# Kernel optimization log

Measured on AMD Instinct MI355X. Metric: run time of the kernel, lower is better.

The kernel has to match this reference:

```python
import jax, jax.numpy as jnp
import numpy as np

VOCAB, D, A, H, F = 100000, 128, 128, 4, 128  # embed dim == attention_dim (residual), 4 heads, final_dim
B, L, L2 = 64, 200, 50
NEG = float(-2**32 + 1)


def setup_inputs() -> dict:
    key = jax.random.key(0)
    ks = jax.random.split(key, 12)
    queries = jax.random.randint(ks[0], (B, L), 0, VOCAB)
    keys = jax.random.randint(ks[1], (B, L, L2), 0, VOCAB)
    E = jax.random.normal(ks[2], (VOCAB, D), dtype=jnp.float32) * 0.02
    Wq = jax.random.normal(ks[3], (D, A), dtype=jnp.float32) * (1.0 / np.sqrt(D))
    bq = jnp.zeros((A,), jnp.float32)
    Wk = jax.random.normal(ks[4], (D, A), dtype=jnp.float32) * (1.0 / np.sqrt(D))
    bk = jnp.zeros((A,), jnp.float32)
    Wv = jax.random.normal(ks[5], (D, A), dtype=jnp.float32) * (1.0 / np.sqrt(D))
    bv = jnp.zeros((A,), jnp.float32)
    Wf = jax.random.normal(ks[6], (A, F), dtype=jnp.float32) * (1.0 / np.sqrt(A))
    bf = jnp.zeros((F,), jnp.float32)
    return {"queries": queries, "keys": keys, "E": E, "Wq": Wq, "bq": bq,
            "Wk": Wk, "bk": bk, "Wv": Wv, "bv": bv, "Wf": Wf, "bf": bf}


def reference(queries, keys, E, Wq, bq, Wk, bk, Wv, bv, Wf, bf):
    q_emb = E[queries]                      # [B, L, D]
    k_emb = E[keys]                         # [B, L, L2, D]
    Q = q_emb @ Wq + bq                     # [B, L, A]
    K = k_emb @ Wk + bk                     # [B, L, L2, A]
    V = k_emb @ Wv + bv                     # [B, L, L2, A]
    d = A // H
    Qh = Q.reshape(Q.shape[0], Q.shape[1], H, d)                       # [B, L, H, d]
    Kh = K.reshape(K.shape[0], K.shape[1], K.shape[2], H, d)           # [B, L, L2, H, d]
    Vh = V.reshape(V.shape[0], V.shape[1], V.shape[2], H, d)
    # per-(b,l) query attends over its L2 keys, per head; scale by sqrt(depth)
    scores = jnp.einsum('blhd,blkhd->bhlk', Qh, Kh) / jnp.sqrt(jnp.asarray(d, Q.dtype))
    # padding mask from embedded-key content: sign(|sum_d k_emb|) == 0 -> masked
    key_mask = jnp.sign(jnp.abs(jnp.sum(k_emb, axis=-1)))              # [B, L, L2]
    scores = jnp.where(key_mask[:, None, :, :] == 0, NEG, scores)
    attn = jax.nn.softmax(scores, axis=-1)                             # [B, H, L, L2]
    out = jnp.einsum('bhlk,blkhd->blhd', attn, Vh)
    out = out.reshape(out.shape[0], out.shape[1], A)                   # [B, L, A]
    out = out + q_emb                                                  # residual
    return out @ Wf + bf                                               # [B, L, F]
```

## Files before the change

### kernel.cpp

```cpp
#include <hip/hip_runtime.h>
#include <stdint.h>

#define DN 128
#define AN 128
#define HN 4
#define FN 128
#define L2N 50
#define NPOS (64*200)
#define NEGC (-4294967295.0f)

#define OFF_MTWB 0
#define OFF_GTB  40960
#define OFF_CB   73728
#define OFF_U    74368
#define OFF_R    3351168
#define OFF_PV   4989568

typedef __fp16 half2v __attribute__((ext_vector_type(2)));
typedef __fp16 f16x8  __attribute__((ext_vector_type(8)));
typedef float  f32x4  __attribute__((ext_vector_type(4)));
union frg { uint4 u; f16x8 h; };

__device__ __forceinline__ float dot2(uint32_t a, uint32_t b, float c) {
#if __has_builtin(__builtin_amdgcn_fdot2)
    union { uint32_t u; half2v h; } ca, cb; ca.u = a; cb.u = b;
    return __builtin_amdgcn_fdot2(ca.h, cb.h, c, false);
#else
    union { uint32_t u; _Float16 h[2]; } ca, cb; ca.u = a; cb.u = b;
    return c + (float)ca.h[0]*(float)cb.h[0] + (float)ca.h[1]*(float)cb.h[1];
#endif
}
__device__ __forceinline__ uint32_t packh2(float x, float y) {
    union { _Float16 h[2]; uint32_t u; } c; c.h[0] = (_Float16)x; c.h[1] = (_Float16)y;
    return c.u;
}
__device__ __forceinline__ float lo16f(uint32_t u) {
    union { uint32_t u; _Float16 h[2]; } c; c.u = u; return (float)c.h[0];
}
__device__ __forceinline__ float hi16f(uint32_t u) {
    union { uint32_t u; _Float16 h[2]; } c; c.u = u; return (float)c.h[1];
}

__global__ __launch_bounds__(256) void k0_pre(
    const float* __restrict__ Wq, const float* __restrict__ bq,
    const float* __restrict__ Wk, const float* __restrict__ bk,
    const float* __restrict__ Wv, const float* __restrict__ bv,
    const float* __restrict__ Wf, const float* __restrict__ bfb,
    float* __restrict__ ws)
{
    uint32_t* MTWB = (uint32_t*)ws + OFF_MTWB;
    uint32_t* GTBw = (uint32_t*)ws + OFF_GTB;
    float*    CB   = ws + OFF_CB;
    const int idx = blockIdx.x*256 + threadIdx.x;

    if (idx < 40960) {
        int jj = idx & 3, lane = (idx>>2)&63, kk = (idx>>8)&3, tn = idx>>10;
        int outc = tn*16 + (lane&15);
        int dd2  = kk*16 + (lane>>4)*4 + jj;
        int dd0  = 2*dd2, dd1 = dd0+1;
        float s0, s1;
        if (outc < 512) {
            int h = outc >> 7, d = outc & 127;
            const float* wk = Wk + d*AN + h*32;
            const float* q0 = Wq + dd0*AN + h*32;
            const float* q1 = Wq + dd1*AN + h*32;
            s0 = 0.f; s1 = 0.f;
            #pragma unroll 8
            for (int j = 0; j < 32; ++j) { float w = wk[j]; s0 += q0[j]*w; s1 += q1[j]*w; }
        } else {
            int f = outc - 512;
            s0 = Wf[dd0*FN + f]; s1 = Wf[dd1*FN + f];
        }
        MTWB[idx] = packh2(s0, s1);
    } else if (idx < 73728) {
        int i2 = idx - 40960;
        int jj = i2 & 3, lane = (i2>>2)&63, kk = (i2>>8)&15, tn = i2>>12;
        int f  = tn*16 + (lane&15);
        int j2 = kk*16 + (lane>>4)*4 + jj;
        int hd0 = 2*j2;
        int h = hd0 >> 7, d0 = hd0 & 127, d1 = d0+1;
        const float* v0 = Wv + d0*AN + h*32;
        const float* v1 = Wv + d1*AN + h*32;
        float s0 = 0.f, s1 = 0.f;
        #pragma unroll 8
        for (int a = 0; a < 32; ++a) {
            float wf = Wf[(h*32+a)*FN + f];
            s0 += v0[a]*wf; s1 += v1[a]*wf;
        }
        GTBw[i2] = packh2(s0, s1);
    } else {
        int c = idx - 73728;
        if (c < 512) {
            int h = c >> 7, d = c & 127;
            float s = 0.f;
            #pragma unroll 8
            for (int j = 0; j < 32; ++j) s += Wk[d*AN + h*32 + j]*bq[h*32 + j];
            CB[c] = s;
        } else if (c < 640) {
            int f = c - 512;
            float s = bfb[f];
            for (int a = 0; a < AN; ++a) s += bv[a]*Wf[a*FN + f];
            CB[c] = s;
        }
    }
}

__global__ __launch_bounds__(256) void k1_proj(
    const int* __restrict__ queries, const float* __restrict__ E,
    float* __restrict__ ws)
{
    const uint32_t* MTWB = (const uint32_t*)ws + OFF_MTWB;
    const float*    CB   = ws + OFF_CB;
    uint32_t* U = (uint32_t*)ws + OFF_U;
    float*    R = ws + OFF_R;

    const int t = threadIdx.x, wv = t >> 6, ln = t & 63;
    const int W  = blockIdx.x*4 + wv;
    const int tm = W / 5, g = W - tm*5;
    const int m = ln & 15, q = ln >> 4;
    const int pos0 = tm*16 + q*4;

    const int qidx = queries[tm*16 + m];
    const float* Eq = E + (size_t)qidx * DN;

    frg a[4];
    #pragma unroll
    for (int kk = 0; kk < 4; ++kk) {
        float4 e0 = *(const float4*)(Eq + kk*32 + q*8);
        float4 e1 = *(const float4*)(Eq + kk*32 + q*8 + 4);
        a[kk].u.x = packh2(e0.x, e0.y);
        a[kk].u.y = packh2(e0.z, e0.w);
        a[kk].u.z = packh2(e1.x, e1.y);
        a[kk].u.w = packh2(e1.z, e1.w);
    }

    #pragma unroll 1
    for (int i = 0; i < 8; ++i) {
        const int tn = g*8 + i;
        const float cb = CB[tn*16 + m];
        f32x4 c = {cb, cb, cb, cb};
        #pragma unroll
        for (int kk = 0; kk < 4; ++kk) {
            frg b; b.u = *(const uint4*)(MTWB + ((size_t)(tn*4 + kk)*64 + ln)*4);
            c = __builtin_amdgcn_mfma_f32_16x16x32_f16(a[kk].h, b.h, c, 0, 0, 0);
        }
        if (tn < 32) {
            float p0 = __shfl_xor(c[0], 1);
            float p1 = __shfl_xor(c[1], 1);
            float p2 = __shfl_xor(c[2], 1);
            float p3 = __shfl_xor(c[3], 1);
            if ((ln & 1) == 0) {
                const int ucol = tn*8 + (m >> 1);
                U[(size_t)(pos0+0)*256 + ucol] = packh2(c[0], p0);
                U[(size_t)(pos0+1)*256 + ucol] = packh2(c[1], p1);
                U[(size_t)(pos0+2)*256 + ucol] = packh2(c[2], p2);
                U[(size_t)(pos0+3)*256 + ucol] = packh2(c[3], p3);
            }
        } else {
            const int f = (tn - 32)*16 + m;
            R[(size_t)(pos0+0)*128 + f] = c[0];
            R[(size_t)(pos0+1)*128 + f] = c[1];
            R[(size_t)(pos0+2)*128 + f] = c[2];
            R[(size_t)(pos0+3)*128 + f] = c[3];
        }
    }
}

__global__ __launch_bounds__(128, 2) void k2_attn(
    const int* __restrict__ keys, const float* __restrict__ E,
    float* __restrict__ ws)
{
    __shared__ __align__(16) uint32_t smem[7748];

    const uint32_t* U  = (const uint32_t*)ws + OFF_U;
    uint32_t*       PV = (uint32_t*)ws + OFF_PV;

    const int t = threadIdx.x, wv = t >> 6, ln = t & 63;
    const int pos = blockIdx.x*2 + wv;
    const int n = ln & 15, qd = ln >> 4;
    const int half = ln >> 5;
    const int m32 = ln & 31;

    uint32_t* kT = smem + wv*3400;
    uint32_t* Us = smem + 6800 + wv*272;
    float*    aT = (float*)(smem + 7344 + wv*200);

    const int* kptr = keys + (size_t)pos*L2N;
    const float* Eg = E + 4*m32;

    const int myk = kptr[ln < L2N ? ln : 0];

    uint4 uv = ((const uint4*)(U + (size_t)pos*256))[ln];

    float4 f4[25];
    #pragma unroll
    for (int i = 0; i < 25; ++i) {
        int row = __shfl(myk, 2*i + half);
        f4[i] = *(const float4*)(Eg + (size_t)row*DN);
    }

    *(uint4*)&Us[qd*68 + (n<<2)] = uv;

    frg bfr[4];
    #pragma unroll
    for (int kk = 0; kk < 4; ++kk) {
        if (n < 4) {
            bfr[kk].u = *(const uint4*)&Us[n*68 + kk*16 + (qd<<2)];
        } else if (n == 4) {
            bfr[kk].u.x = 0x3C003C00u; bfr[kk].u.y = 0x3C003C00u;
            bfr[kk].u.z = 0x3C003C00u; bfr[kk].u.w = 0x3C003C00u;
        } else {
            bfr[kk].u.x = 0u; bfr[kk].u.y = 0u; bfr[kk].u.z = 0u; bfr[kk].u.w = 0u;
        }
    }

    f32x4 c[4];
    #pragma unroll
    for (int mt = 0; mt < 4; ++mt) {
        const int icnt = (mt == 3) ? 1 : 8;
        #pragma unroll
        for (int ii = 0; ii < 8; ++ii) {
            if (ii < icnt) {
                const int i = mt*8 + ii;
                const int key = 2*i + half;
                float4 cur = f4[i];
                uint32_t p0 = packh2(cur.x, cur.y);
                uint32_t p1 = packh2(cur.z, cur.w);
                *(uint2*)&kT[key*68 + 2*m32] = (uint2){p0, p1};
            }
        }
        c[mt] = (f32x4){0.f, 0.f, 0.f, 0.f};
        #pragma unroll
        for (int kk = 0; kk < 4; ++kk) {
            frg a; a.u = *(const uint4*)&kT[(mt*16 + n)*68 + kk*16 + (qd<<2)];
            c[mt] = __builtin_amdgcn_mfma_f32_16x16x32_f16(a.h, bfr[kk].h, c[mt], 0, 0, 0);
        }
    }

    {
        float sc[4][4];
        float mx = -__builtin_inff();
        #pragma unroll
        for (int mt = 0; mt < 4; ++mt) {
            #pragma unroll
            for (int j = 0; j < 4; ++j) {
                float ksv = __shfl(c[mt][j], (ln & 48) | 4);
                float v = c[mt][j] * 0.17677669529663687f;
                v = (ksv == 0.0f) ? NEGC : v;
                int key = mt*16 + (qd<<2) + j;
                if (key >= L2N) v = -__builtin_inff();
                sc[mt][j] = v;
                mx = fmaxf(mx, v);
            }
        }
        mx = fmaxf(mx, __shfl_xor(mx, 16));
        mx = fmaxf(mx, __shfl_xor(mx, 32));
        float e[4][4];
        float sum = 0.f;
        #pragma unroll
        for (int mt = 0; mt < 4; ++mt) {
            #pragma unroll
            for (int j = 0; j < 4; ++j) {
                float ev = __expf(sc[mt][j] - mx);
                e[mt][j] = ev; sum += ev;
            }
        }
        sum += __shfl_xor(sum, 16);
        sum += __shfl_xor(sum, 32);
        const float inv = 1.0f / sum;
        if (n < 4) {
            #pragma unroll
            for (int mt = 0; mt < 4; ++mt) {
                #pragma unroll
                for (int j = 0; j < 4; ++j) {
                    int key = mt*16 + (qd<<2) + j;
                    if (key < L2N) aT[key*4 + n] = e[mt][j] * inv;
                }
            }
        }
    }

    {
        float pa0=0.f,pb0=0.f,pa1=0.f,pb1=0.f,pa2=0.f,pb2=0.f,pa3=0.f,pb3=0.f;
        #pragma unroll
        for (int r = 0; r < L2N; ++r) {
            float4 w4 = *(const float4*)&aT[r*4];
            uint32_t kp = kT[r*68 + ln];
            float kx = lo16f(kp), ky = hi16f(kp);
            pa0 += w4.x*kx; pb0 += w4.x*ky;
            pa1 += w4.y*kx; pb1 += w4.y*ky;
            pa2 += w4.z*kx; pb2 += w4.z*ky;
            pa3 += w4.w*kx; pb3 += w4.w*ky;
        }
        uint32_t* PVp = PV + (size_t)pos*256;
        PVp[0*64 + ln] = packh2(pa0, pb0);
        PVp[1*64 + ln] = packh2(pa1, pb1);
        PVp[2*64 + ln] = packh2(pa2, pb2);
        PVp[3*64 + ln] = packh2(pa3, pb3);
    }
}

__global__ __launch_bounds__(256) void k3_out(
    const float* __restrict__ ws, float* __restrict__ out)
{
    const uint32_t* GTB = (const uint32_t*)ws + OFF_GTB;
    const uint32_t* PV  = (const uint32_t*)ws + OFF_PV;
    const float*    R   = ws + OFF_R;

    const int t = threadIdx.x, wv = t >> 6, ln = t & 63;
    const int W  = blockIdx.x*4 + wv;
    const int tm = W >> 2, g = W & 3;
    const int m = ln & 15, q = ln >> 4;
    const int pos0 = tm*16 + q*4;

    frg a[16];
    const uint32_t* PVa = PV + (size_t)(tm*16 + m)*256;
    #pragma unroll
    for (int kk = 0; kk < 16; ++kk)
        a[kk].u = *(const uint4*)(PVa + kk*16 + q*4);

    #pragma unroll 1
    for (int i = 0; i < 2; ++i) {
        const int nt = g*2 + i;
        const int f = nt*16 + m;
        f32x4 c;
        c[0] = R[(size_t)(pos0+0)*128 + f];
        c[1] = R[(size_t)(pos0+1)*128 + f];
        c[2] = R[(size_t)(pos0+2)*128 + f];
        c[3] = R[(size_t)(pos0+3)*128 + f];
        #pragma unroll
        for (int kk = 0; kk < 16; ++kk) {
            frg b; b.u = *(const uint4*)(GTB + ((size_t)(nt*16 + kk)*64 + ln)*4);
            c = __builtin_amdgcn_mfma_f32_16x16x32_f16(a[kk].h, b.h, c, 0, 0, 0);
        }
        out[(size_t)(pos0+0)*128 + f] = c[0];
        out[(size_t)(pos0+1)*128 + f] = c[1];
        out[(size_t)(pos0+2)*128 + f] = c[2];
        out[(size_t)(pos0+3)*128 + f] = c[3];
    }
}

extern "C" void kernel_launch(void* const* d_in, const int* in_sizes, int n_in,
                              void* d_out, int out_size, void* d_ws, size_t ws_size,
                              hipStream_t stream) {
    const int* queries = (const int*)d_in[0];
    const int* keys    = (const int*)d_in[1];
    const float* E   = (const float*)d_in[2];
    const float* Wq  = (const float*)d_in[3];
    const float* bq  = (const float*)d_in[4];
    const float* Wk  = (const float*)d_in[5];
    const float* bk  = (const float*)d_in[6];
    const float* Wv  = (const float*)d_in[7];
    const float* bv  = (const float*)d_in[8];
    const float* Wf  = (const float*)d_in[9];
    const float* bfb = (const float*)d_in[10];
    float* ws = (float*)d_ws;
    float* o  = (float*)d_out;

    hipLaunchKernelGGL(k0_pre,  dim3(291),  dim3(256), 0, stream,
                       Wq, bq, Wk, bk, Wv, bv, Wf, bfb, ws);
    hipLaunchKernelGGL(k1_proj, dim3(1000), dim3(256), 0, stream, queries, E, ws);
    hipLaunchKernelGGL(k2_attn, dim3(6400), dim3(128), 0, stream, keys, E, ws);
    hipLaunchKernelGGL(k3_out,  dim3(800),  dim3(256), 0, stream, ws, o);
}
```

Before: 179.6 us.

## Pre-convert embedding table to fp16 and gather half-width rows in attention

Adds a kernel that converts the full fp32 embedding table to fp16 in workspace on every call. A new attention kernel gathers 8-byte fp16 key rows instead of 16-byte fp32 rows, which halves the gather traffic. It also uses less shared memory and allows higher occupancy (launch bounds of 4 blocks). The trade-off is an extra full-table read and write per call, and the new path only runs if the workspace is large enough.

```diff
diff --git a/kernel.cpp b/kernel.cpp
--- a/kernel.cpp
+++ b/kernel.cpp
@@ -15,21 +15,13 @@
 #define OFF_U    74368
 #define OFF_R    3351168
 #define OFF_PV   4989568
+#define OFF_EH   8266368
 
 typedef __fp16 half2v __attribute__((ext_vector_type(2)));
 typedef __fp16 f16x8  __attribute__((ext_vector_type(8)));
 typedef float  f32x4  __attribute__((ext_vector_type(4)));
 union frg { uint4 u; f16x8 h; };
 
-__device__ __forceinline__ float dot2(uint32_t a, uint32_t b, float c) {
-#if __has_builtin(__builtin_amdgcn_fdot2)
-    union { uint32_t u; half2v h; } ca, cb; ca.u = a; cb.u = b;
-    return __builtin_amdgcn_fdot2(ca.h, cb.h, c, false);
-#else
-    union { uint32_t u; _Float16 h[2]; } ca, cb; ca.u = a; cb.u = b;
-    return c + (float)ca.h[0]*(float)cb.h[0] + (float)ca.h[1]*(float)cb.h[1];
-#endif
-}
 __device__ __forceinline__ uint32_t packh2(float x, float y) {
     union { _Float16 h[2]; uint32_t u; } c; c.h[0] = (_Float16)x; c.h[1] = (_Float16)y;
     return c.u;
@@ -39,6 +31,19 @@
 }
 __device__ __forceinline__ float hi16f(uint32_t u) {
     union { uint32_t u; _Float16 h[2]; } c; c.u = u; return (float)c.h[1];
+}
+
+__global__ __launch_bounds__(256) void k_ecvt(
+    const float* __restrict__ E, uint32_t* __restrict__ EH)
+{
+    const int tid = blockIdx.x*256 + threadIdx.x;
+    const int stride = gridDim.x*256;
+    const int total = 100000*32;
+    for (int i = tid; i < total; i += stride) {
+        float4 v = ((const float4*)E)[i];
+        uint2 p; p.x = packh2(v.x, v.y); p.y = packh2(v.z, v.w);
+        ((uint2*)EH)[i] = p;
+    }
 }
 
 __global__ __launch_bounds__(256) void k0_pre(
@@ -166,6 +171,155 @@
     }
 }
 
+__global__ __launch_bounds__(128, 4) void k2_attn_h(
+    const int* __restrict__ keys, const uint32_t* __restrict__ EH,
+    float* __restrict__ ws)
+{
+    __shared__ __align__(16) uint32_t smem[3120];
+
+    const uint32_t* U  = (const uint32_t*)ws + OFF_U;
+    uint32_t*       PV = (uint32_t*)ws + OFF_PV;
+
+    const int t = threadIdx.x, wv = t >> 6, ln = t & 63;
+    const int pos = blockIdx.x*2 + wv;
+    const int n = ln & 15, qd = ln >> 4;
+    const int half = ln >> 5;
+    const int m32 = ln & 31;
+
+    uint32_t* kT = smem + wv*1560;
+    uint32_t* Us = smem + wv*1560 + 1088;
+    float*    aT = (float*)(smem + wv*1560 + 1360);
+
+    const int* kptr = keys + (size_t)pos*L2N;
+
+    const int myk = kptr[ln < L2N ? ln : 0];
+
+    uint4 uv = ((const uint4*)(U + (size_t)pos*256))[ln];
+
+    uint2 f2[25];
+    #pragma unroll
+    for (int i = 0; i < 25; ++i) {
+        int row = __shfl(myk, 2*i + half);
+        f2[i] = *(const uint2*)(EH + (size_t)row*64 + 2*m32);
+    }
+    #pragma unroll
+    for (int i = 0; i < 25; ++i)
+        asm volatile("" : "+v"(f2[i].x), "+v"(f2[i].y));
+
+    *(uint4*)&Us[qd*68 + (n<<2)] = uv;
+
+    frg bfr[4];
+    #pragma unroll
+    for (int kk = 0; kk < 4; ++kk) {
+        if (n < 4) {
+            bfr[kk].u = *(const uint4*)&Us[n*68 + kk*16 + (qd<<2)];
+        } else if (n == 4) {
+            bfr[kk].u.x = 0x3C003C00u; bfr[kk].u.y = 0x3C003C00u;
+            bfr[kk].u.z = 0x3C003C00u; bfr[kk].u.w = 0x3C003C00u;
+        } else {
+            bfr[kk].u.x = 0u; bfr[kk].u.y = 0u; bfr[kk].u.z = 0u; bfr[kk].u.w = 0u;
+        }
+    }
+
+    f32x4 c[4];
+    #pragma unroll
+    for (int mt = 0; mt < 4; ++mt) {
+        const int icnt = (mt == 3) ? 1 : 8;
+        #pragma unroll
+        for (int ii = 0; ii < 8; ++ii) {
+            if (ii < icnt) {
+                const int i = mt*8 + ii;
+                const int lk = 2*ii + half;
+                *(uint2*)&kT[lk*68 + 2*m32] = f2[i];
+            }
+        }
+        c[mt] = (f32x4){0.f, 0.f, 0.f, 0.f};
+        #pragma unroll
+        for (int kk = 0; kk < 4; ++kk) {
+            frg a; a.u = *(const uint4*)&kT[n*68 + kk*16 + (qd<<2)];
+            c[mt] = __builtin_amdgcn_mfma_f32_16x16x32_f16(a.h, bfr[kk].h, c[mt], 0, 0, 0);
+        }
+    }
+
+    {
+        float sc[4][4];
+        float mx = -__builtin_inff();
+        #pragma unroll
+        for (int mt = 0; mt < 4; ++mt) {
+            #pragma unroll
+            for (int j = 0; j < 4; ++j) {
+                float ksv = __shfl(c[mt][j], (ln & 48) | 4);
+                float v = c[mt][j] * 0.17677669529663687f;
+                v = (ksv == 0.0f) ? NEGC : v;
+                int key = mt*16 + (qd<<2) + j;
+                if (key >= L2N) v = -__builtin_inff();
+                sc[mt][j] = v;
+                mx = fmaxf(mx, v);
+            }
+        }
+        mx = fmaxf(mx, __shfl_xor(mx, 16));
+        mx = fmaxf(mx, __shfl_xor(mx, 32));
+        float e[4][4];
+        float sum = 0.f;
+        #pragma unroll
+        for (int mt = 0; mt < 4; ++mt) {
+            #pragma unroll
+            for (int j = 0; j < 4; ++j) {
+                float ev = __expf(sc[mt][j] - mx);
+                e[mt][j] = ev; sum += ev;
+            }
+        }
+        sum += __shfl_xor(sum, 16);
+        sum += __shfl_xor(sum, 32);
+        const float inv = 1.0f / sum;
+        if (n < 4) {
+            #pragma unroll
+            for (int mt = 0; mt < 4; ++mt) {
+                #pragma unroll
+                for (int j = 0; j < 4; ++j) {
+                    int key = mt*16 + (qd<<2) + j;
+                    if (key < L2N) aT[key*4 + n] = e[mt][j] * inv;
+                }
+            }
+        }
+    }
+
+    {
+        float p[4][4];
+        #pragma unroll
+        for (int h = 0; h < 4; ++h)
+            #pragma unroll
+            for (int d = 0; d < 4; ++d) p[h][d] = 0.f;
+
+        #pragma unroll
+        for (int i = 0; i < 25; ++i) {
+            const int key = 2*i + half;
+            float4 w4 = *(const float4*)&aT[key*4];
+            float k0 = lo16f(f2[i].x), k1v = hi16f(f2[i].x);
+            float k2v = lo16f(f2[i].y), k3v = hi16f(f2[i].y);
+            p[0][0] += w4.x*k0; p[0][1] += w4.x*k1v; p[0][2] += w4.x*k2v; p[0][3] += w4.x*k3v;
+            p[1][0] += w4.y*k0; p[1][1] += w4.y*k1v; p[1][2] += w4.y*k2v; p[1][3] += w4.y*k3v;
+            p[2][0] += w4.z*k0; p[2][1] += w4.z*k1v; p[2][2] += w4.z*k2v; p[2][3] += w4.z*k3v;
+            p[3][0] += w4.w*k0; p[3][1] += w4.w*k1v; p[3][2] += w4.w*k2v; p[3][3] += w4.w*k3v;
+        }
+        #pragma unroll
+        for (int h = 0; h < 4; ++h)
+            #pragma unroll
+            for (int d = 0; d < 4; ++d)
+                p[h][d] += __shfl_xor(p[h][d], 32);
+
+        float a0 = half ? p[2][0] : p[0][0], a1 = half ? p[2][1] : p[0][1];
+        float a2 = half ? p[2][2] : p[0][2], a3 = half ? p[2][3] : p[0][3];
+        float b0 = half ? p[3][0] : p[1][0], b1 = half ? p[3][1] : p[1][1];
+        float b2 = half ? p[3][2] : p[1][2], b3 = half ? p[3][3] : p[1][3];
+
+        uint32_t* PVp = PV + (size_t)pos*256;
+        const int hA = 2*half, hB = 2*half + 1;
+        *(uint2*)&PVp[hA*64 + 2*m32] = (uint2){ packh2(a0, a1), packh2(a2, a3) };
+        *(uint2*)&PVp[hB*64 + 2*m32] = (uint2){ packh2(b0, b1), packh2(b2, b3) };
+    }
+}
+
 __global__ __launch_bounds__(128, 2) void k2_attn(
     const int* __restrict__ keys, const float* __restrict__ E,
     float* __restrict__ ws)
@@ -189,7 +343,6 @@
     const float* Eg = E + 4*m32;
 
     const int myk = kptr[ln < L2N ? ln : 0];
-
     uint4 uv = ((const uint4*)(U + (size_t)pos*256))[ln];
 
     float4 f4[25];
@@ -357,9 +510,21 @@
     float* ws = (float*)d_ws;
     float* o  = (float*)d_out;
 
+    const size_t need = ((size_t)OFF_EH + 100000ull*64ull) * 4ull;
+    const bool useEH = (ws_size >= need);
+
+    if (useEH) {
+        hipLaunchKernelGGL(k_ecvt, dim3(2048), dim3(256), 0, stream,
+                           E, (uint32_t*)ws + OFF_EH);
+    }
     hipLaunchKernelGGL(k0_pre,  dim3(291),  dim3(256), 0, stream,
                        Wq, bq, Wk, bk, Wv, bv, Wf, bfb, ws);
     hipLaunchKernelGGL(k1_proj, dim3(1000), dim3(256), 0, stream, queries, E, ws);
-    hipLaunchKernelGGL(k2_attn, dim3(6400), dim3(128), 0, stream, keys, E, ws);
+    if (useEH) {
+        hipLaunchKernelGGL(k2_attn_h, dim3(6400), dim3(128), 0, stream,
+                           keys, (const uint32_t*)ws + OFF_EH, ws);
+    } else {
+        hipLaunchKernelGGL(k2_attn, dim3(6400), dim3(128), 0, stream, keys, E, ws);
+    }
     hipLaunchKernelGGL(k3_out,  dim3(800),  dim3(256), 0, stream, ws, o);
 }
```

Result: faster. 171.7 us (-4.4%).
